# Optimization experiments

Hardware: AMD Instinct MI355X
Metric: run time of the kernel (lower is better)

## Reference

```python
import jax, jax.numpy as jnp
import numpy as np

L, D, N_HEADS = 4096, 1024, 16
HEAD_D = D // N_HEADS


def setup_inputs() -> dict:
    key = jax.random.key(0)
    kx, kq, kbq, ko, kbo = jax.random.split(key, 5)
    lim_in = 1.0 / np.sqrt(D)
    return {
        "x": jax.random.normal(kx, (L, D), dtype=jnp.float32),
        # equinox nn.Linear(dim, 3*dim): weight [3D, D], bias [3D], uniform(-1/sqrt(in), 1/sqrt(in))
        "W_qkv": jax.random.uniform(kq, (3 * D, D), jnp.float32, -lim_in, lim_in),
        "b_qkv": jax.random.uniform(kbq, (3 * D,), jnp.float32, -lim_in, lim_in),
        "W_out": jax.random.uniform(ko, (D, D), jnp.float32, -lim_in, lim_in),
        "b_out": jax.random.uniform(kbo, (D,), jnp.float32, -lim_in, lim_in),
    }


def reference(x, W_qkv, b_qkv, W_out, b_out):
    # qkv projection: equinox Linear computes W @ x + b per token -> x @ W.T + b
    qkv = x @ W_qkv.T + b_qkv                         # [L, 3D]
    qkv = qkv.reshape(L, 3, N_HEADS, HEAD_D)
    qkv = jnp.transpose(qkv, (1, 2, 0, 3))            # [3, n, L, d]
    q, k, v = qkv[0], qkv[1], qkv[2]                  # each [n, L, d]

    scale = 1.0 / jnp.sqrt(jnp.asarray(HEAD_D, dtype=x.dtype))
    attn = jnp.einsum('nqd,nkd->nqk', q, k) * scale   # [n, L, L]
    causal = jnp.tril(jnp.ones((L, L), dtype=bool))
    attn = jnp.where(causal, attn, -jnp.inf)
    attn = jax.nn.softmax(attn, axis=-1)              # dropout rate 0 -> identity
    out = jnp.einsum('nqk,nkd->nqd', attn, v)         # [n, L, d]
    out = jnp.transpose(out, (1, 0, 2)).reshape(L, D)
    return out @ W_out.T + b_out                      # [L, D]
```

## Files before the change

### kernel.cpp

```cpp
#include <hip/hip_runtime.h>
#include <hip/hip_bf16.h>
#include <math.h>

#define L_SEQ 4096
#define DIM   1024
#define NH    16
#define HD    64

#define QSCL 0.18033688011112042f

typedef __attribute__((ext_vector_type(4)))  float f32x4;
typedef __attribute__((ext_vector_type(16))) float f32x16;
typedef __attribute__((ext_vector_type(8)))  short s16x8;
typedef __attribute__((ext_vector_type(4)))  short s16x4;
typedef __attribute__((ext_vector_type(4)))  unsigned u32x4;

__device__ __forceinline__ short f2bf(float f) {
  unsigned u = __builtin_bit_cast(unsigned, f);
  u = u + 0x7fffu + ((u >> 16) & 1u);
  return (short)(u >> 16);
}

__device__ __forceinline__ unsigned cvt_pk_bf16(float lo, float hi_) {
  unsigned r;
  asm("v_cvt_pk_bf16_f32 %0, %1, %2" : "=v"(r) : "v"(lo), "v"(hi_));
  return r;
}

__device__ __forceinline__ float exp2_fast(float x) {
  float r;
  asm("v_exp_f32 %0, %1" : "=v"(r) : "v"(x));
  return r;
}

__device__ __forceinline__ void gload_lds16(const void* g, void* l) {
  __builtin_amdgcn_global_load_lds(
      (__attribute__((address_space(1))) void*)(g),
      (__attribute__((address_space(3))) void*)(l), 16, 0, 0);
}

__global__ __launch_bounds__(256) void cvt_f32_bf16(const float* __restrict__ src,
                                                    short* __restrict__ dst, int n4) {
  int i = blockIdx.x * 256 + threadIdx.x;
  if (i >= n4) return;
  f32x4 f = *(const f32x4*)(src + i * 4);
  s16x4 o;
  o[0] = f2bf(f[0]); o[1] = f2bf(f[1]); o[2] = f2bf(f[2]); o[3] = f2bf(f[3]);
  *(s16x4*)(dst + i * 4) = o;
}


#define GEMM_MAINLOOP(A_, B_, Kdim)                                            \
  f32x4 acc[4][4];                                                             \
  _Pragma("unroll") for (int m = 0; m < 4; ++m)                                \
  _Pragma("unroll") for (int n = 0; n < 4; ++n) acc[m][n] = (f32x4)0.f;        \
  const short* aptr = A_ + (bm * 128 + w * 16 + (l >> 2)) * (Kdim) + (l & 3) * 8; \
  const short* bptr = B_ + (bn * 128 + w * 16 + (l >> 2)) * (Kdim) + (l & 3) * 8; \
  short* asl = &As[(w * 16) * 32];                                             \
  short* bsl = &Bs[(w * 16) * 32];                                             \
  for (int kk = 0; kk < (Kdim); kk += 32) {                                    \
    gload_lds16(aptr + kk, asl);                                               \
    gload_lds16(aptr + kk + 64 * (Kdim), asl + 64 * 32);                       \
    gload_lds16(bptr + kk, bsl);                                               \
    gload_lds16(bptr + kk + 64 * (Kdim), bsl + 64 * 32);                       \
    __syncthreads();                                                           \
    s16x8 af[4], bfr[4];                                                       \
    _Pragma("unroll") for (int m = 0; m < 4; ++m)                              \
      af[m] = *(const s16x8*)&As[(wr * 64 + m * 16 + lr) * 32 + lg * 8];       \
    _Pragma("unroll") for (int n = 0; n < 4; ++n)                              \
      bfr[n] = *(const s16x8*)&Bs[(wc * 64 + n * 16 + lr) * 32 + lg * 8];      \
    _Pragma("unroll") for (int m = 0; m < 4; ++m)                              \
    _Pragma("unroll") for (int n = 0; n < 4; ++n)                              \
      acc[m][n] = __builtin_amdgcn_mfma_f32_16x16x32_bf16(af[m], bfr[n], acc[m][n], 0, 0, 0); \
    __syncthreads();                                                           \
  }

__global__ __launch_bounds__(256) void gemm_qkv(const short* __restrict__ A,
                                                const short* __restrict__ B,
                                                const float* __restrict__ bias,
                                                short* __restrict__ Qb,
                                                short* __restrict__ Kf,
                                                short* __restrict__ Vf) {
  __shared__ __align__(16) short As[128 * 32];
  __shared__ __align__(16) short Bs[128 * 32];
  const int t = threadIdx.x;
  const int w = t >> 6, l = t & 63;
  const int wr = w >> 1, wc = w & 1;
  const int lr = l & 15, lg = l >> 4;
  const int bm = blockIdx.x, bn = blockIdx.y;

  GEMM_MAINLOOP(A, B, DIM)

  const int row0 = bm * 128 + wr * 64;
  const int col0 = bn * 128 + wc * 64;
#pragma unroll
  for (int n = 0; n < 4; ++n) {
    const int col = col0 + n * 16 + lr;
    const float bv = bias[col];
    const int which = col >> 10;
    const int head = (col & 1023) >> 6;
    const int d = col & 63;
    if (which == 0) {
      short* dst = Qb + (head * L_SEQ) * HD + d;
#pragma unroll
      for (int m = 0; m < 4; ++m)
#pragma unroll
        for (int j = 0; j < 4; ++j) {
          const int row = row0 + m * 16 + lg * 4 + j;
          dst[row * HD] = f2bf((acc[m][n][j] + bv) * QSCL);
        }
    } else if (which == 1) {
      const int c = d >> 4, khi = (d >> 3) & 1, e = d & 7;
      short* dst = Kf + head * (L_SEQ * HD);
#pragma unroll
      for (int m = 0; m < 4; ++m)
#pragma unroll
        for (int j = 0; j < 4; ++j) {
          const int row = row0 + m * 16 + lg * 4 + j;
          const int p = row >> 5;
          const int lane = khi * 32 + (row & 31);
          dst[((p * 4 + c) * 64 + lane) * 8 + e] = f2bf(acc[m][n][j] + bv);
        }
    } else {
      const int dh = d >> 5;
      const int dq = d & 31;
      short* dst = Vf + head * (L_SEQ * HD);
#pragma unroll
      for (int m = 0; m < 4; ++m) {
        const int rowb = row0 + m * 16 + lg * 4;
        const int tt = rowb >> 6;
        const int kc = (rowb >> 4) & 3;
        const int khi = (rowb >> 3) & 1;
        const int e0 = rowb & 7;
        s16x4 wv;
#pragma unroll
        for (int j = 0; j < 4; ++j) wv[j] = f2bf(acc[m][n][j] + bv);
        *(s16x4*)&dst[(((tt * 4 + kc) * 2 + dh) * 64 + khi * 32 + dq) * 8 + e0] = wv;
      }
    }
  }
}

__global__ __launch_bounds__(256) void gemm_out(const short* __restrict__ A,
                                                const short* __restrict__ B,
                                                const float* __restrict__ bias,
                                                float* __restrict__ C) {
  __shared__ __align__(16) short As[128 * 32];
  __shared__ __align__(16) short Bs[128 * 32];
  const int t = threadIdx.x;
  const int w = t >> 6, l = t & 63;
  const int wr = w >> 1, wc = w & 1;
  const int lr = l & 15, lg = l >> 4;
  const int bm = blockIdx.x, bn = blockIdx.y;

  GEMM_MAINLOOP(A, B, DIM)

  const int row0 = bm * 128 + wr * 64;
  const int col0 = bn * 128 + wc * 64;
#pragma unroll
  for (int n = 0; n < 4; ++n) {
    const int col = col0 + n * 16 + lr;
    const float bv = bias[col];
#pragma unroll
    for (int m = 0; m < 4; ++m)
#pragma unroll
      for (int j = 0; j < 4; ++j) {
        const int row = row0 + m * 16 + lg * 4 + j;
        C[row * DIM + col] = acc[m][n][j] + bv;
      }
  }
}

__global__ __launch_bounds__(128, 4) void attn32(const short* __restrict__ Qb,
                                                 const short* __restrict__ Kf,
                                                 const short* __restrict__ Vf,
                                                 short* __restrict__ Ob) {
  __shared__ float Mg[64 * 33];
  const int bid = blockIdx.x;
  const int xcd = bid & 7;
  const int idx = bid >> 3;
  const int head = (xcd << 1) | (idx & 1);
  const int qt = idx >> 1;
  const int qtile = (qt & 1) ? (qt >> 1) : (127 - (qt >> 1));
  const int q0 = qtile * 32;
  const int h = threadIdx.x >> 6;
  const int l = threadIdx.x & 63;
  const int q = l & 31;
  const int hi = l >> 5;

  const short* Qh = Qb + head * (L_SEQ * HD);
  const short* Kh = Kf + head * (L_SEQ * HD);
  const short* Vh = Vf + head * (L_SEQ * HD);

  s16x8 qf[4];
#pragma unroll
  for (int c = 0; c < 4; ++c)
    qf[c] = *(const s16x8*)&Qh[(q0 + q) * HD + c * 16 + hi * 8];

  f32x16 o0 = (f32x16)0.f, o1 = (f32x16)0.f;
  f32x4 lvec = (f32x4)0.f;

  const int nkt = qtile + 1;

  s16x8 kf[4];
#pragma unroll
  for (int c = 0; c < 4; ++c)
    kf[c] = *(const s16x8*)&Kh[((h * 4 + c) * 64 + l) * 8];

  for (int kt = h; kt < nkt; kt += 2) {
    s16x8 vf[2][2];
#pragma unroll
    for (int cc = 0; cc < 2; ++cc)
#pragma unroll
      for (int dh = 0; dh < 2; ++dh)
        vf[cc][dh] = *(const s16x8*)
            &Vh[((((kt >> 1) * 4 + (kt & 1) * 2 + cc) * 2 + dh) * 64 + l) * 8];

    f32x16 s = (f32x16)0.f;
#pragma unroll
    for (int c = 0; c < 4; ++c)
      s = __builtin_amdgcn_mfma_f32_32x32x16_bf16(kf[c], qf[c], s, 0, 0, 0);

    const int ktn = (kt + 2 < nkt) ? kt + 2 : kt;
#pragma unroll
    for (int c = 0; c < 4; ++c)
      kf[c] = *(const s16x8*)&Kh[((ktn * 4 + c) * 64 + l) * 8];

    if (kt == qtile) {
      const int qrel = q - hi * 4;
#pragma unroll
      for (int r = 0; r < 16; ++r) {
        const int koff = (r & 3) + 8 * (r >> 2);
        if (koff > qrel) s[r] = -1e30f;
      }
    }

#pragma unroll
    for (int r = 0; r < 16; ++r) s[r] = exp2_fast(s[r]);
#pragma unroll
    for (int r = 0; r < 16; ++r) lvec[r & 3] += s[r];

#pragma unroll
    for (int cc = 0; cc < 2; ++cc) {
      const int roff = cc * 8;
      const unsigned A = cvt_pk_bf16(s[roff + 0], s[roff + 1]);
      const unsigned B = cvt_pk_bf16(s[roff + 2], s[roff + 3]);
      const unsigned C = cvt_pk_bf16(s[roff + 4], s[roff + 5]);
      const unsigned D = cvt_pk_bf16(s[roff + 6], s[roff + 7]);
      const unsigned sA = (unsigned)__shfl_xor((int)A, 32, 64);
      const unsigned sB = (unsigned)__shfl_xor((int)B, 32, 64);
      const unsigned sC = (unsigned)__shfl_xor((int)C, 32, 64);
      const unsigned sD = (unsigned)__shfl_xor((int)D, 32, 64);
      u32x4 pw;
      pw[0] = hi ? sC : A;
      pw[1] = hi ? sD : B;
      pw[2] = hi ? C : sA;
      pw[3] = hi ? D : sB;
      const s16x8 pf = __builtin_bit_cast(s16x8, pw);
      o0 = __builtin_amdgcn_mfma_f32_32x32x16_bf16(vf[cc][0], pf, o0, 0, 0, 0);
      o1 = __builtin_amdgcn_mfma_f32_32x32x16_bf16(vf[cc][1], pf, o1, 0, 0, 0);
    }
  }

  float lsum = (lvec[0] + lvec[1]) + (lvec[2] + lvec[3]);
  lsum += __shfl_xor(lsum, 32, 64);

  if (h == 0) {
    float* st = &Mg[l * 33];
    st[0] = lsum;
#pragma unroll
    for (int r = 0; r < 16; ++r) { st[1 + r] = o0[r]; st[17 + r] = o1[r]; }
  }
  __syncthreads();
  if (h == 1) {
    const float* st = &Mg[l * 33];
    const float inv = 1.f / (st[0] + lsum);
    const int orow = q0 + q;
#pragma unroll
    for (int dh = 0; dh < 2; ++dh) {
#pragma unroll
      for (int tq = 0; tq < 4; ++tq) {
        s16x4 wv;
#pragma unroll
        for (int j = 0; j < 4; ++j) {
          const int r = tq * 4 + j;
          const float ov = (dh == 0) ? (st[1 + r] + o0[r]) : (st[17 + r] + o1[r]);
          wv[j] = f2bf(ov * inv);
        }
        *(s16x4*)&Ob[orow * DIM + head * HD + dh * 32 + tq * 8 + hi * 4] = wv;
      }
    }
  }
}

extern "C" void kernel_launch(void* const* d_in, const int* in_sizes, int n_in,
                              void* d_out, int out_size, void* d_ws, size_t ws_size,
                              hipStream_t stream) {
  const float* x    = (const float*)d_in[0];
  const float* Wqkv = (const float*)d_in[1];
  const float* bqkv = (const float*)d_in[2];
  const float* Wout = (const float*)d_in[3];
  const float* bout = (const float*)d_in[4];
  float* out = (float*)d_out;

  char* ws = (char*)d_ws;
  short* xb    = (short*)(ws);
  short* wqkvb = (short*)(ws + (8u  << 20));
  short* woutb = (short*)(ws + (14u << 20));
  short* Qb    = (short*)(ws + (16u << 20));
  short* Kf    = (short*)(ws + (24u << 20));
  short* Vf    = (short*)(ws + (32u << 20));
  short* Ob    = (short*)(ws + (40u << 20));

  cvt_f32_bf16<<<(L_SEQ * DIM / 4 + 255) / 256, 256, 0, stream>>>(x, xb, L_SEQ * DIM / 4);
  cvt_f32_bf16<<<(3 * DIM * DIM / 4 + 255) / 256, 256, 0, stream>>>(Wqkv, wqkvb, 3 * DIM * DIM / 4);
  cvt_f32_bf16<<<(DIM * DIM / 4 + 255) / 256, 256, 0, stream>>>(Wout, woutb, DIM * DIM / 4);

  gemm_qkv<<<dim3(L_SEQ / 128, 3 * DIM / 128), 256, 0, stream>>>(xb, wqkvb, bqkv, Qb, Kf, Vf);
  attn32<<<2048, 128, 0, stream>>>(Qb, Kf, Vf, Ob);
  gemm_out<<<dim3(L_SEQ / 128, DIM / 128), 256, 0, stream>>>(Ob, woutb, bout, out);
}
```

Before: 144.5 us.

## Split attention KV loop across four waves with bf16 LDS merge and MFMA priority

The attention block grows from two to four wavefronts, so each wave handles every fourth key tile. This shortens the per-block serial KV loop and adds latency hiding. Partial outputs from waves 1-3 are packed to bf16 in LDS and summed by wave 0, which cuts shared-memory size but rounds the partial sums. The MFMA sections are wrapped in s_setprio to favour matrix issue. The V indexing is rewritten to match, assuming V is stored in a plain per-tile layout, and the short last tiles leave some waves idle in small blocks.

```diff
diff --git a/kernel.cpp b/kernel.cpp
--- a/kernel.cpp
+++ b/kernel.cpp
@@ -171,11 +171,11 @@
   }
 }
 
-__global__ __launch_bounds__(128, 4) void attn32(const short* __restrict__ Qb,
+__global__ __launch_bounds__(256, 4) void attn32(const short* __restrict__ Qb,
                                                  const short* __restrict__ Kf,
                                                  const short* __restrict__ Vf,
                                                  short* __restrict__ Ob) {
-  __shared__ float Mg[64 * 33];
+  __shared__ unsigned Ms[3][64][17];
   const int bid = blockIdx.x;
   const int xcd = bid & 7;
   const int idx = bid >> 3;
@@ -207,21 +207,22 @@
   for (int c = 0; c < 4; ++c)
     kf[c] = *(const s16x8*)&Kh[((h * 4 + c) * 64 + l) * 8];
 
-  for (int kt = h; kt < nkt; kt += 2) {
+  for (int kt = h; kt < nkt; kt += 4) {
     s16x8 vf[2][2];
 #pragma unroll
     for (int cc = 0; cc < 2; ++cc)
 #pragma unroll
       for (int dh = 0; dh < 2; ++dh)
-        vf[cc][dh] = *(const s16x8*)
-            &Vh[((((kt >> 1) * 4 + (kt & 1) * 2 + cc) * 2 + dh) * 64 + l) * 8];
+        vf[cc][dh] = *(const s16x8*)&Vh[(((kt * 2 + cc) * 2 + dh) * 64 + l) * 8];
 
     f32x16 s = (f32x16)0.f;
+    __builtin_amdgcn_s_setprio(1);
 #pragma unroll
     for (int c = 0; c < 4; ++c)
       s = __builtin_amdgcn_mfma_f32_32x32x16_bf16(kf[c], qf[c], s, 0, 0, 0);
-
-    const int ktn = (kt + 2 < nkt) ? kt + 2 : kt;
+    __builtin_amdgcn_s_setprio(0);
+
+    const int ktn = (kt + 4 < nkt) ? kt + 4 : kt;
 #pragma unroll
     for (int c = 0; c < 4; ++c)
       kf[c] = *(const s16x8*)&Kh[((ktn * 4 + c) * 64 + l) * 8];
@@ -257,24 +258,41 @@
       pw[2] = hi ? C : sA;
       pw[3] = hi ? D : sB;
       const s16x8 pf = __builtin_bit_cast(s16x8, pw);
+      __builtin_amdgcn_s_setprio(1);
       o0 = __builtin_amdgcn_mfma_f32_32x32x16_bf16(vf[cc][0], pf, o0, 0, 0, 0);
       o1 = __builtin_amdgcn_mfma_f32_32x32x16_bf16(vf[cc][1], pf, o1, 0, 0, 0);
+      __builtin_amdgcn_s_setprio(0);
     }
   }
 
   float lsum = (lvec[0] + lvec[1]) + (lvec[2] + lvec[3]);
   lsum += __shfl_xor(lsum, 32, 64);
 
+  if (h > 0) {
+    unsigned* st = &Ms[h - 1][l][0];
+#pragma unroll
+    for (int w2 = 0; w2 < 8; ++w2) st[w2]     = cvt_pk_bf16(o0[2 * w2], o0[2 * w2 + 1]);
+#pragma unroll
+    for (int w2 = 0; w2 < 8; ++w2) st[8 + w2] = cvt_pk_bf16(o1[2 * w2], o1[2 * w2 + 1]);
+    st[16] = __builtin_bit_cast(unsigned, lsum);
+  }
+  __syncthreads();
   if (h == 0) {
-    float* st = &Mg[l * 33];
-    st[0] = lsum;
-#pragma unroll
-    for (int r = 0; r < 16; ++r) { st[1 + r] = o0[r]; st[17 + r] = o1[r]; }
-  }
-  __syncthreads();
-  if (h == 1) {
-    const float* st = &Mg[l * 33];
-    const float inv = 1.f / (st[0] + lsum);
+#pragma unroll
+    for (int wv = 0; wv < 3; ++wv) {
+      const unsigned* st = &Ms[wv][l][0];
+      lsum += __builtin_bit_cast(float, st[16]);
+#pragma unroll
+      for (int w2 = 0; w2 < 8; ++w2) {
+        const unsigned ua = st[w2];
+        o0[2 * w2]     += __builtin_bit_cast(float, ua << 16);
+        o0[2 * w2 + 1] += __builtin_bit_cast(float, ua & 0xffff0000u);
+        const unsigned ub = st[8 + w2];
+        o1[2 * w2]     += __builtin_bit_cast(float, ub << 16);
+        o1[2 * w2 + 1] += __builtin_bit_cast(float, ub & 0xffff0000u);
+      }
+    }
+    const float inv = 1.f / lsum;
     const int orow = q0 + q;
 #pragma unroll
     for (int dh = 0; dh < 2; ++dh) {
@@ -284,7 +302,7 @@
 #pragma unroll
         for (int j = 0; j < 4; ++j) {
           const int r = tq * 4 + j;
-          const float ov = (dh == 0) ? (st[1 + r] + o0[r]) : (st[17 + r] + o1[r]);
+          const float ov = (dh == 0) ? o0[r] : o1[r];
           wv[j] = f2bf(ov * inv);
         }
         *(s16x4*)&Ob[orow * DIM + head * HD + dh * 32 + tq * 8 + hi * 4] = wv;
@@ -317,6 +335,6 @@
   cvt_f32_bf16<<<(DIM * DIM / 4 + 255) / 256, 256, 0, stream>>>(Wout, woutb, DIM * DIM / 4);
 
   gemm_qkv<<<dim3(L_SEQ / 128, 3 * DIM / 128), 256, 0, stream>>>(xb, wqkvb, bqkv, Qb, Kf, Vf);
-  attn32<<<2048, 128, 0, stream>>>(Qb, Kf, Vf, Ob);
+  attn32<<<2048, 256, 0, stream>>>(Qb, Kf, Vf, Ob);
   gemm_out<<<dim3(L_SEQ / 128, DIM / 128), 256, 0, stream>>>(Ob, woutb, bout, out);
 }
```

After: 144.3 us. Within noise of the previous version (-0.1%).
